# Performance work log

Measured on AMD Instinct MI355X. Metric: run time of the kernel, lower is better.

## Reference

```python
import jax, jax.numpy as jnp
import numpy as np

N = 8192
D = 256
DENSITY = 0.02  # ~164 neighbors per node


def setup_inputs() -> dict:
    key = jax.random.key(0)
    k1, k2, k3, k4 = jax.random.split(key, 4)
    inputs = jax.random.normal(k1, (N, D), dtype=jnp.float32)
    vals = jax.random.uniform(k2, (N, N), dtype=jnp.float32, minval=0.1, maxval=1.0)
    mask = jax.random.uniform(k3, (N, N), dtype=jnp.float32) < DENSITY
    adj = jnp.where(mask, vals, 0.0)
    H_v = 0.1 * jax.random.normal(k4, (D, 1), dtype=jnp.float32)
    return {"inputs": inputs, "adj": adj, "H_v": H_v}


def reference(inputs, adj, H_v):
    # scores[j] = inputs[j] . H_v  -> sparse values v_ij = adj_ij * scores[j]
    scores = jnp.squeeze(inputs @ H_v, -1)            # [N]
    mask = adj != 0.0                                  # nonzero pattern of SparseTensor
    logits = adj * scores[None, :]                     # [N, N]
    neg = jnp.asarray(jnp.finfo(logits.dtype).min, logits.dtype)
    logits = jnp.where(mask, logits, neg)
    # sparse softmax: normalize only over nonzero entries per row
    m = jnp.max(logits, axis=1, keepdims=True)
    e = jnp.where(mask, jnp.exp(logits - m), 0.0)
    s = jnp.sum(e, axis=1, keepdims=True)
    weights = e / jnp.where(s > 0, s, 1.0)             # empty rows -> all-zero weights
    # sparse_tensor_dense_matmul(weights, inputs)
    return weights @ inputs                            # [N, D]
```

## Files before the change

kernel.cpp:

```cpp
#include <hip/hip_runtime.h>

#define NN 8192
#define DD 256
#define RCAP 512

typedef float v4f __attribute__((ext_vector_type(4)));
typedef unsigned short u16x4 __attribute__((ext_vector_type(4)));

__device__ __forceinline__ unsigned short f2bf_rne(float x) {
    unsigned u = __float_as_uint(x);
    u += 0x7fffu + ((u >> 16) & 1u);
    return (unsigned short)(u >> 16);
}

__device__ __forceinline__ float4 bf4_to_f4(u16x4 u) {
    float4 r;
    r.x = __uint_as_float((unsigned)u.x << 16);
    r.y = __uint_as_float((unsigned)u.y << 16);
    r.z = __uint_as_float((unsigned)u.z << 16);
    r.w = __uint_as_float((unsigned)u.w << 16);
    return r;
}

template <bool WRITE_IB>
__global__ __launch_bounds__(256) void prep_kernel(const float* __restrict__ inputs,
                                                   const float* __restrict__ Hv,
                                                   float* __restrict__ scores,
                                                   unsigned short* __restrict__ ib) {
    int wave = threadIdx.x >> 6;
    int lane = threadIdx.x & 63;
    int row  = blockIdx.x * 4 + wave;
    float4 v = ((const float4*)(inputs + (size_t)row * DD))[lane];
    if (WRITE_IB) {
        u16x4 u;
        u.x = f2bf_rne(v.x); u.y = f2bf_rne(v.y); u.z = f2bf_rne(v.z); u.w = f2bf_rne(v.w);
        ((u16x4*)(ib + (size_t)row * DD))[lane] = u;
    }
    float4 h = ((const float4*)Hv)[lane];
    float s = v.x * h.x + v.y * h.y + v.z * h.z + v.w * h.w;
    #pragma unroll
    for (int off = 32; off > 0; off >>= 1) s += __shfl_down(s, off, 64);
    if (lane == 0) scores[row] = s;
}


__device__ __forceinline__ void process_row(const v4f a[8], int row, int tid, int lane, int wave,
                                            const float* __restrict__ scores,
                                            float2* __restrict__ csr, int* __restrict__ cnt,
                                            float2* s_ja, int* s_wsum) {
    int nz = 0;
#pragma unroll
    for (int c = 0; c < 8; ++c)
        nz += (a[c].x != 0.f) + (a[c].y != 0.f) + (a[c].z != 0.f) + (a[c].w != 0.f);

    int pre = nz;
#pragma unroll
    for (int off = 1; off < 64; off <<= 1) {
        int t = __shfl_up(pre, off, 64);
        if (lane >= off) pre += t;
    }
    if (lane == 63) s_wsum[wave] = pre;
    __syncthreads();
    int base = 0, total = 0;
#pragma unroll
    for (int w = 0; w < 4; ++w) {
        int t = s_wsum[w];
        if (w < wave) base += t;
        total += t;
    }

    int off = base + pre - nz;
#pragma unroll
    for (int c = 0; c < 8; ++c) {
        int j0 = c * 1024 + tid * 4;
        float v;
        v = a[c].x; if (v != 0.f) { if (off < RCAP) s_ja[off] = make_float2(__int_as_float(j0 + 0), v); off++; }
        v = a[c].y; if (v != 0.f) { if (off < RCAP) s_ja[off] = make_float2(__int_as_float(j0 + 1), v); off++; }
        v = a[c].z; if (v != 0.f) { if (off < RCAP) s_ja[off] = make_float2(__int_as_float(j0 + 2), v); off++; }
        v = a[c].w; if (v != 0.f) { if (off < RCAP) s_ja[off] = make_float2(__int_as_float(j0 + 3), v); off++; }
    }
    __syncthreads();

    int lim = total <= RCAP ? total : RCAP;
    for (int k = tid; k < lim; k += 256) {
        float2 ja = s_ja[k];
        int j = __float_as_int(ja.x);
        float e = __expf(ja.y * scores[j]);
        csr[(size_t)row * RCAP + k] = make_float2(ja.x, e);
    }
    if (tid == 0) cnt[row] = total;
    __syncthreads();
}

__global__ __launch_bounds__(256) void build_kernel(const float* __restrict__ adj,
                                                    const float* __restrict__ scores,
                                                    float2* __restrict__ csr,
                                                    int* __restrict__ cnt) {
    __shared__ float2 s_ja[RCAP];
    __shared__ int s_wsum[4];

    const int tid  = threadIdx.x;
    const int lane = tid & 63;
    const int wave = tid >> 6;
    const int row0 = blockIdx.x * 2;

    const v4f* p0 = (const v4f*)(adj + (size_t)row0 * NN);
    const v4f* p1 = (const v4f*)(adj + (size_t)(row0 + 1) * NN);
    v4f a0[8], a1[8];
#pragma unroll
    for (int c = 0; c < 8; ++c) a0[c] = __builtin_nontemporal_load(&p0[c * 256 + tid]);
#pragma unroll
    for (int c = 0; c < 8; ++c) a1[c] = __builtin_nontemporal_load(&p1[c * 256 + tid]);

    process_row(a0, row0,     tid, lane, wave, scores, csr, cnt, s_ja, s_wsum);
    process_row(a1, row0 + 1, tid, lane, wave, scores, csr, cnt, s_ja, s_wsum);
}


__device__ __forceinline__ void batch8(const unsigned short* __restrict__ ib,
                                       int jl, int el, int m, int lane4,
                                       float4& acc, float& ssum) {
    int js[8]; float es[8]; float4 f[8];
#pragma unroll
    for (int u = 0; u < 8; ++u) {
        js[u] = __builtin_amdgcn_readlane(jl, m + u);
        es[u] = __uint_as_float(__builtin_amdgcn_readlane(el, m + u));
    }
#pragma unroll
    for (int u = 0; u < 8; ++u)
        f[u] = bf4_to_f4(*(const u16x4*)(ib + (size_t)js[u] * DD + lane4));
#pragma unroll
    for (int u = 0; u < 8; ++u) {
        acc.x += es[u] * f[u].x; acc.y += es[u] * f[u].y;
        acc.z += es[u] * f[u].z; acc.w += es[u] * f[u].w;
        ssum  += es[u];
    }
}

__device__ void gather_pair(const float2* __restrict__ eA, int bA, int keA,
                            const float2* __restrict__ eB, int bB, int keB,
                            const unsigned short* __restrict__ ib,
                            int lane, int lane4,
                            float4& accA, float& ssA, float4& accB, float& ssB) {
    while (bA < keA || bB < keB) {
        int nA = keA - bA; nA = nA > 64 ? 64 : nA;
        int nB = keB - bB; nB = nB > 64 ? 64 : nB;
        int jlA = 0, elA = 0, jlB = 0, elB = 0;
        if (nA > 0) {
            float2 je = eA[bA + (lane < nA ? lane : 0)];
            if (lane >= nA) je.y = 0.f;
            jlA = __float_as_int(je.x); elA = __float_as_int(je.y);
        }
        if (nB > 0) {
            float2 je = eB[bB + (lane < nB ? lane : 0)];
            if (lane >= nB) je.y = 0.f;
            jlB = __float_as_int(je.x); elB = __float_as_int(je.y);
        }
        int nA8 = nA > 0 ? ((nA + 7) & ~7) : 0;
        int nB8 = nB > 0 ? ((nB + 7) & ~7) : 0;
        int mx = nA8 > nB8 ? nA8 : nB8;
        for (int m = 0; m < mx; m += 8) {
            if (m < nA8) batch8(ib, jlA, elA, m, lane4, accA, ssA);
            if (m < nB8) batch8(ib, jlB, elB, m, lane4, accB, ssB);
        }
        if (nA > 0) bA += nA;
        if (nB > 0) bB += nB;
    }
}

__device__ void slow_row(const float* __restrict__ adj, int row,
                         const float* __restrict__ scores,
                         const unsigned short* __restrict__ ib,
                         float2* s_je, int* s_cnt,
                         int tid, int lane, int lane4, int wave,
                         float4& acc, float& ssum) {
    const float* arow = adj + (size_t)row * NN;
    for (int c = 0; c < 8; ++c) {
        if (tid == 0) *s_cnt = 0;
        __syncthreads();
        float4 a = ((const float4*)(arow + c * 1024))[tid];
        int j0 = c * 1024 + tid * 4;
        float v;
        v = a.x; if (v != 0.f) { int k = atomicAdd(s_cnt, 1); s_je[k] = make_float2(__int_as_float(j0 + 0), __expf(v * scores[j0 + 0])); }
        v = a.y; if (v != 0.f) { int k = atomicAdd(s_cnt, 1); s_je[k] = make_float2(__int_as_float(j0 + 1), __expf(v * scores[j0 + 1])); }
        v = a.z; if (v != 0.f) { int k = atomicAdd(s_cnt, 1); s_je[k] = make_float2(__int_as_float(j0 + 2), __expf(v * scores[j0 + 2])); }
        v = a.w; if (v != 0.f) { int k = atomicAdd(s_cnt, 1); s_je[k] = make_float2(__int_as_float(j0 + 3), __expf(v * scores[j0 + 3])); }
        __syncthreads();
        int tc = *s_cnt;
        float4 dummy = make_float4(0.f, 0.f, 0.f, 0.f); float sdummy = 0.f;
        gather_pair(s_je, wave * tc / 4, (wave + 1) * tc / 4,
                    s_je, 0, 0, ib, lane, lane4, acc, ssum, dummy, sdummy);
        __syncthreads();
    }
}

__global__ __launch_bounds__(256) void gather_kernel(const float2* __restrict__ csr,
                                                     const int* __restrict__ cnt,
                                                     const unsigned short* __restrict__ ib,
                                                     const float* __restrict__ adj,
                                                     const float* __restrict__ scores,
                                                     float* __restrict__ out) {
    __shared__ float  s_red[2][4 * DD];
    __shared__ float  s_ss[2][4];
    __shared__ float2 s_je[1024];
    __shared__ int    s_cnt;

    const int tid   = threadIdx.x;
    const int lane  = tid & 63;
    const int wave  = tid >> 6;
    const int lane4 = lane * 4;
    const int row0  = blockIdx.x * 2;
    const int row1  = row0 + 1;

    int t0 = cnt[row0];
    int t1 = cnt[row1];
    float4 acc0 = make_float4(0.f, 0.f, 0.f, 0.f), acc1 = acc0;
    float ss0 = 0.f, ss1 = 0.f;

    if (t0 <= RCAP && t1 <= RCAP) {
        gather_pair(csr + (size_t)row0 * RCAP, wave * t0 / 4, (wave + 1) * t0 / 4,
                    csr + (size_t)row1 * RCAP, wave * t1 / 4, (wave + 1) * t1 / 4,
                    ib, lane, lane4, acc0, ss0, acc1, ss1);
    } else {
        if (t0 <= RCAP) {
            float4 d = make_float4(0.f, 0.f, 0.f, 0.f); float sd = 0.f;
            gather_pair(csr + (size_t)row0 * RCAP, wave * t0 / 4, (wave + 1) * t0 / 4,
                        csr, 0, 0, ib, lane, lane4, acc0, ss0, d, sd);
        } else {
            slow_row(adj, row0, scores, ib, s_je, &s_cnt, tid, lane, lane4, wave, acc0, ss0);
        }
        if (t1 <= RCAP) {
            float4 d = make_float4(0.f, 0.f, 0.f, 0.f); float sd = 0.f;
            gather_pair(csr + (size_t)row1 * RCAP, wave * t1 / 4, (wave + 1) * t1 / 4,
                        csr, 0, 0, ib, lane, lane4, acc1, ss1, d, sd);
        } else {
            slow_row(adj, row1, scores, ib, s_je, &s_cnt, tid, lane, lane4, wave, acc1, ss1);
        }
    }

    if (lane == 0) { s_ss[0][wave] = ss0; s_ss[1][wave] = ss1; }
    *(float4*)&s_red[0][wave * DD + lane4] = acc0;
    *(float4*)&s_red[1][wave * DD + lane4] = acc1;
    __syncthreads();
    float tot0 = s_ss[0][0] + s_ss[0][1] + s_ss[0][2] + s_ss[0][3];
    float tot1 = s_ss[1][0] + s_ss[1][1] + s_ss[1][2] + s_ss[1][3];
    float r0 = s_red[0][0 * DD + tid] + s_red[0][1 * DD + tid] + s_red[0][2 * DD + tid] + s_red[0][3 * DD + tid];
    float r1 = s_red[1][0 * DD + tid] + s_red[1][1 * DD + tid] + s_red[1][2 * DD + tid] + s_red[1][3 * DD + tid];
    out[(size_t)row0 * DD + tid] = (tot0 > 0.f) ? r0 / tot0 : 0.f;
    out[(size_t)row1 * DD + tid] = (tot1 > 0.f) ? r1 / tot1 : 0.f;
}

__global__ __launch_bounds__(256) void attn_fallback(const float* __restrict__ adj,
                                                     const float* __restrict__ inputs,
                                                     const float* __restrict__ scores,
                                                     float* __restrict__ out) {
    __shared__ int   s_j[1024];
    __shared__ float s_e[1024];
    __shared__ int   s_cnt;
    const int row = blockIdx.x;
    const int tid = threadIdx.x;
    const float* arow = adj + (size_t)row * NN;
    float acc = 0.f, ssum = 0.f;
    for (int base = 0; base < NN; base += 1024) {
        if (tid == 0) s_cnt = 0;
        __syncthreads();
        float4 a = ((const float4*)(arow + base))[tid];
        int j0 = base + tid * 4;
        if (a.x != 0.f) { int k = atomicAdd(&s_cnt, 1); s_j[k] = j0 + 0; s_e[k] = __expf(a.x * scores[j0 + 0]); }
        if (a.y != 0.f) { int k = atomicAdd(&s_cnt, 1); s_j[k] = j0 + 1; s_e[k] = __expf(a.y * scores[j0 + 1]); }
        if (a.z != 0.f) { int k = atomicAdd(&s_cnt, 1); s_j[k] = j0 + 2; s_e[k] = __expf(a.z * scores[j0 + 2]); }
        if (a.w != 0.f) { int k = atomicAdd(&s_cnt, 1); s_j[k] = j0 + 3; s_e[k] = __expf(a.w * scores[j0 + 3]); }
        __syncthreads();
        int c = s_cnt;
        for (int k = 0; k < c; ++k) {
            float e = s_e[k];
            acc  += e * inputs[(size_t)s_j[k] * DD + tid];
            ssum += e;
        }
        __syncthreads();
    }
    out[(size_t)row * DD + tid] = (ssum > 0.f) ? acc / ssum : 0.f;
}

extern "C" void kernel_launch(void* const* d_in, const int* in_sizes, int n_in,
                              void* d_out, int out_size, void* d_ws, size_t ws_size,
                              hipStream_t stream) {
    const float* inputs = (const float*)d_in[0];
    const float* adj    = (const float*)d_in[1];
    const float* Hv     = (const float*)d_in[2];
    float* out = (float*)d_out;

    char* ws = (char*)d_ws;
    float*          scores = (float*)ws;
    unsigned short* ib     = (unsigned short*)(ws + 32768);
    int*            cnt    = (int*)(ws + 32768 + (size_t)NN * DD * 2);
    float2*         csr    = (float2*)(ws + 65536 + (size_t)NN * DD * 2);

    const size_t need = 65536 + (size_t)NN * DD * 2 + (size_t)NN * RCAP * sizeof(float2);

    if (ws_size >= need) {
        prep_kernel<true><<<NN / 4, 256, 0, stream>>>(inputs, Hv, scores, ib);
        build_kernel<<<NN / 2, 256, 0, stream>>>(adj, scores, csr, cnt);
        gather_kernel<<<NN / 2, 256, 0, stream>>>(csr, cnt, ib, adj, scores, out);
    } else {
        prep_kernel<false><<<NN / 4, 256, 0, stream>>>(inputs, Hv, scores, nullptr);
        attn_fallback<<<NN, 256, 0, stream>>>(adj, inputs, scores, out);
    }
}
```

Before: 399.4 us.

## Fuse CSR build and gather into one per-row kernel using shared-memory neighbor lists

Merges the separate build and gather kernels into a single kernel with one block per row. Each block compacts the row's nonzeros and their exp weights into shared memory and gathers bf16 neighbor rows from there directly, so the global CSR buffer is never written or read back. The gather now has each half-wave load 8 bf16 values per lane from a different neighbor, and the shared-memory capacity is raised to 1024 entries. In exchange there is a larger shared-memory reduction, each block handles only one row instead of two, and there is less overlap between the adjacency stream and the gather.

```diff
diff --git a/kernel.cpp b/kernel.cpp
--- a/kernel.cpp
+++ b/kernel.cpp
@@ -2,24 +2,16 @@
 
 #define NN 8192
 #define DD 256
-#define RCAP 512
+#define RCAP 1024
 
 typedef float v4f __attribute__((ext_vector_type(4)));
 typedef unsigned short u16x4 __attribute__((ext_vector_type(4)));
+typedef unsigned short u16x8 __attribute__((ext_vector_type(8)));
 
 __device__ __forceinline__ unsigned short f2bf_rne(float x) {
     unsigned u = __float_as_uint(x);
     u += 0x7fffu + ((u >> 16) & 1u);
     return (unsigned short)(u >> 16);
-}
-
-__device__ __forceinline__ float4 bf4_to_f4(u16x4 u) {
-    float4 r;
-    r.x = __uint_as_float((unsigned)u.x << 16);
-    r.y = __uint_as_float((unsigned)u.y << 16);
-    r.z = __uint_as_float((unsigned)u.z << 16);
-    r.w = __uint_as_float((unsigned)u.w << 16);
-    return r;
 }
 
 template <bool WRITE_IB>
@@ -43,16 +35,81 @@
     if (lane == 0) scores[row] = s;
 }
 
-
-__device__ __forceinline__ void process_row(const v4f a[8], int row, int tid, int lane, int wave,
-                                            const float* __restrict__ scores,
-                                            float2* __restrict__ csr, int* __restrict__ cnt,
-                                            float2* s_ja, int* s_wsum) {
+__device__ __forceinline__ void batch8x2(const unsigned short* __restrict__ ib,
+                                         int jl, int el, int m, int sel, int lane8,
+                                         float4& accL, float4& accH, float& ssum) {
+    int js[8]; float es[8];
+#pragma unroll
+    for (int u = 0; u < 8; ++u) {
+        js[u] = __builtin_amdgcn_readlane(jl, m + u);
+        es[u] = __uint_as_float(__builtin_amdgcn_readlane(el, m + u));
+    }
+    u16x8 g[4];
+#pragma unroll
+    for (int p = 0; p < 4; ++p) {
+        int j = sel ? js[2 * p + 1] : js[2 * p];
+        g[p] = *(const u16x8*)(ib + (size_t)j * DD + lane8);
+    }
+#pragma unroll
+    for (int p = 0; p < 4; ++p) {
+        float e = sel ? es[2 * p + 1] : es[2 * p];
+        float4 lo, hi;
+        lo.x = __uint_as_float((unsigned)g[p][0] << 16);
+        lo.y = __uint_as_float((unsigned)g[p][1] << 16);
+        lo.z = __uint_as_float((unsigned)g[p][2] << 16);
+        lo.w = __uint_as_float((unsigned)g[p][3] << 16);
+        hi.x = __uint_as_float((unsigned)g[p][4] << 16);
+        hi.y = __uint_as_float((unsigned)g[p][5] << 16);
+        hi.z = __uint_as_float((unsigned)g[p][6] << 16);
+        hi.w = __uint_as_float((unsigned)g[p][7] << 16);
+        accL.x += e * lo.x; accL.y += e * lo.y; accL.z += e * lo.z; accL.w += e * lo.w;
+        accH.x += e * hi.x; accH.y += e * hi.y; accH.z += e * hi.z; accH.w += e * hi.w;
+        ssum += e;
+    }
+}
+
+__device__ __forceinline__ void gather_range(const float2* __restrict__ s_je, int b, int ke,
+                                             const unsigned short* __restrict__ ib, int lane,
+                                             float4& accL, float4& accH, float& ssum) {
+    const int sel   = lane >> 5;
+    const int lane8 = (lane & 31) * 8;
+    while (b < ke) {
+        int n = ke - b; n = n > 64 ? 64 : n;
+        float2 je = s_je[b + (lane < n ? lane : 0)];
+        if (lane >= n) je.y = 0.f;
+        int jl = __float_as_int(je.x);
+        int el = __float_as_int(je.y);
+        int n8 = (n + 7) & ~7;
+        for (int m = 0; m < n8; m += 8)
+            batch8x2(ib, jl, el, m, sel, lane8, accL, accH, ssum);
+        b += n;
+    }
+}
+
+__global__ __launch_bounds__(256) void fused_kernel(const float* __restrict__ adj,
+                                                    const float* __restrict__ scores,
+                                                    const unsigned short* __restrict__ ib,
+                                                    float* __restrict__ out) {
+    __shared__ float2 s_je[RCAP];
+    __shared__ float  s_red[8 * DD];
+    __shared__ float  s_ss[8];
+    __shared__ int    s_wsum[4];
+    __shared__ int    s_cnt;
+
+    const int tid  = threadIdx.x;
+    const int lane = tid & 63;
+    const int wave = tid >> 6;
+    const int row  = blockIdx.x;
+
+    const v4f* p = (const v4f*)(adj + (size_t)row * NN);
+    v4f a[8];
+#pragma unroll
+    for (int c = 0; c < 8; ++c) a[c] = __builtin_nontemporal_load(&p[c * 256 + tid]);
+
     int nz = 0;
 #pragma unroll
     for (int c = 0; c < 8; ++c)
         nz += (a[c].x != 0.f) + (a[c].y != 0.f) + (a[c].z != 0.f) + (a[c].w != 0.f);
-
     int pre = nz;
 #pragma unroll
     for (int off = 1; off < 64; off <<= 1) {
@@ -69,185 +126,52 @@
         total += t;
     }
 
-    int off = base + pre - nz;
-#pragma unroll
-    for (int c = 0; c < 8; ++c) {
-        int j0 = c * 1024 + tid * 4;
-        float v;
-        v = a[c].x; if (v != 0.f) { if (off < RCAP) s_ja[off] = make_float2(__int_as_float(j0 + 0), v); off++; }
-        v = a[c].y; if (v != 0.f) { if (off < RCAP) s_ja[off] = make_float2(__int_as_float(j0 + 1), v); off++; }
-        v = a[c].z; if (v != 0.f) { if (off < RCAP) s_ja[off] = make_float2(__int_as_float(j0 + 2), v); off++; }
-        v = a[c].w; if (v != 0.f) { if (off < RCAP) s_ja[off] = make_float2(__int_as_float(j0 + 3), v); off++; }
-    }
+    float4 accL = make_float4(0.f, 0.f, 0.f, 0.f), accH = accL;
+    float ssum = 0.f;
+
+    if (total <= RCAP) {
+        int off = base + pre - nz;
+#pragma unroll
+        for (int c = 0; c < 8; ++c) {
+            int j0 = c * 1024 + tid * 4;
+            float v;
+            v = a[c].x; if (v != 0.f) { s_je[off] = make_float2(__int_as_float(j0 + 0), __expf(v * scores[j0 + 0])); off++; }
+            v = a[c].y; if (v != 0.f) { s_je[off] = make_float2(__int_as_float(j0 + 1), __expf(v * scores[j0 + 1])); off++; }
+            v = a[c].z; if (v != 0.f) { s_je[off] = make_float2(__int_as_float(j0 + 2), __expf(v * scores[j0 + 2])); off++; }
+            v = a[c].w; if (v != 0.f) { s_je[off] = make_float2(__int_as_float(j0 + 3), __expf(v * scores[j0 + 3])); off++; }
+        }
+        __syncthreads();
+        gather_range(s_je, wave * total / 4, (wave + 1) * total / 4, ib, lane, accL, accH, ssum);
+    } else {
+        for (int c = 0; c < 8; ++c) {
+            if (tid == 0) s_cnt = 0;
+            __syncthreads();
+            int j0 = c * 1024 + tid * 4;
+            float v;
+            v = a[c].x; if (v != 0.f) { int k = atomicAdd(&s_cnt, 1); s_je[k] = make_float2(__int_as_float(j0 + 0), __expf(v * scores[j0 + 0])); }
+            v = a[c].y; if (v != 0.f) { int k = atomicAdd(&s_cnt, 1); s_je[k] = make_float2(__int_as_float(j0 + 1), __expf(v * scores[j0 + 1])); }
+            v = a[c].z; if (v != 0.f) { int k = atomicAdd(&s_cnt, 1); s_je[k] = make_float2(__int_as_float(j0 + 2), __expf(v * scores[j0 + 2])); }
+            v = a[c].w; if (v != 0.f) { int k = atomicAdd(&s_cnt, 1); s_je[k] = make_float2(__int_as_float(j0 + 3), __expf(v * scores[j0 + 3])); }
+            __syncthreads();
+            int tc = s_cnt;
+            gather_range(s_je, wave * tc / 4, (wave + 1) * tc / 4, ib, lane, accL, accH, ssum);
+            __syncthreads();
+        }
+    }
+
+    const int half = wave * 2 + (lane >> 5);
+    const int l8   = (lane & 31) * 8;
+    if ((lane & 31) == 0) s_ss[half] = ssum;
+    *(float4*)&s_red[half * DD + l8]     = accL;
+    *(float4*)&s_red[half * DD + l8 + 4] = accH;
     __syncthreads();
-
-    int lim = total <= RCAP ? total : RCAP;
-    for (int k = tid; k < lim; k += 256) {
-        float2 ja = s_ja[k];
-        int j = __float_as_int(ja.x);
-        float e = __expf(ja.y * scores[j]);
-        csr[(size_t)row * RCAP + k] = make_float2(ja.x, e);
-    }
-    if (tid == 0) cnt[row] = total;
-    __syncthreads();
-}
-
-__global__ __launch_bounds__(256) void build_kernel(const float* __restrict__ adj,
-                                                    const float* __restrict__ scores,
-                                                    float2* __restrict__ csr,
-                                                    int* __restrict__ cnt) {
-    __shared__ float2 s_ja[RCAP];
-    __shared__ int s_wsum[4];
-
-    const int tid  = threadIdx.x;
-    const int lane = tid & 63;
-    const int wave = tid >> 6;
-    const int row0 = blockIdx.x * 2;
-
-    const v4f* p0 = (const v4f*)(adj + (size_t)row0 * NN);
-    const v4f* p1 = (const v4f*)(adj + (size_t)(row0 + 1) * NN);
-    v4f a0[8], a1[8];
-#pragma unroll
-    for (int c = 0; c < 8; ++c) a0[c] = __builtin_nontemporal_load(&p0[c * 256 + tid]);
-#pragma unroll
-    for (int c = 0; c < 8; ++c) a1[c] = __builtin_nontemporal_load(&p1[c * 256 + tid]);
-
-    process_row(a0, row0,     tid, lane, wave, scores, csr, cnt, s_ja, s_wsum);
-    process_row(a1, row0 + 1, tid, lane, wave, scores, csr, cnt, s_ja, s_wsum);
-}
-
-
-__device__ __forceinline__ void batch8(const unsigned short* __restrict__ ib,
-                                       int jl, int el, int m, int lane4,
-                                       float4& acc, float& ssum) {
-    int js[8]; float es[8]; float4 f[8];
-#pragma unroll
-    for (int u = 0; u < 8; ++u) {
-        js[u] = __builtin_amdgcn_readlane(jl, m + u);
-        es[u] = __uint_as_float(__builtin_amdgcn_readlane(el, m + u));
-    }
-#pragma unroll
-    for (int u = 0; u < 8; ++u)
-        f[u] = bf4_to_f4(*(const u16x4*)(ib + (size_t)js[u] * DD + lane4));
-#pragma unroll
-    for (int u = 0; u < 8; ++u) {
-        acc.x += es[u] * f[u].x; acc.y += es[u] * f[u].y;
-        acc.z += es[u] * f[u].z; acc.w += es[u] * f[u].w;
-        ssum  += es[u];
-    }
-}
-
-__device__ void gather_pair(const float2* __restrict__ eA, int bA, int keA,
-                            const float2* __restrict__ eB, int bB, int keB,
-                            const unsigned short* __restrict__ ib,
-                            int lane, int lane4,
-                            float4& accA, float& ssA, float4& accB, float& ssB) {
-    while (bA < keA || bB < keB) {
-        int nA = keA - bA; nA = nA > 64 ? 64 : nA;
-        int nB = keB - bB; nB = nB > 64 ? 64 : nB;
-        int jlA = 0, elA = 0, jlB = 0, elB = 0;
-        if (nA > 0) {
-            float2 je = eA[bA + (lane < nA ? lane : 0)];
-            if (lane >= nA) je.y = 0.f;
-            jlA = __float_as_int(je.x); elA = __float_as_int(je.y);
-        }
-        if (nB > 0) {
-            float2 je = eB[bB + (lane < nB ? lane : 0)];
-            if (lane >= nB) je.y = 0.f;
-            jlB = __float_as_int(je.x); elB = __float_as_int(je.y);
-        }
-        int nA8 = nA > 0 ? ((nA + 7) & ~7) : 0;
-        int nB8 = nB > 0 ? ((nB + 7) & ~7) : 0;
-        int mx = nA8 > nB8 ? nA8 : nB8;
-        for (int m = 0; m < mx; m += 8) {
-            if (m < nA8) batch8(ib, jlA, elA, m, lane4, accA, ssA);
-            if (m < nB8) batch8(ib, jlB, elB, m, lane4, accB, ssB);
-        }
-        if (nA > 0) bA += nA;
-        if (nB > 0) bB += nB;
-    }
-}
-
-__device__ void slow_row(const float* __restrict__ adj, int row,
-                         const float* __restrict__ scores,
-                         const unsigned short* __restrict__ ib,
-                         float2* s_je, int* s_cnt,
-                         int tid, int lane, int lane4, int wave,
-                         float4& acc, float& ssum) {
-    const float* arow = adj + (size_t)row * NN;
-    for (int c = 0; c < 8; ++c) {
-        if (tid == 0) *s_cnt = 0;
-        __syncthreads();
-        float4 a = ((const float4*)(arow + c * 1024))[tid];
-        int j0 = c * 1024 + tid * 4;
-        float v;
-        v = a.x; if (v != 0.f) { int k = atomicAdd(s_cnt, 1); s_je[k] = make_float2(__int_as_float(j0 + 0), __expf(v * scores[j0 + 0])); }
-        v = a.y; if (v != 0.f) { int k = atomicAdd(s_cnt, 1); s_je[k] = make_float2(__int_as_float(j0 + 1), __expf(v * scores[j0 + 1])); }
-        v = a.z; if (v != 0.f) { int k = atomicAdd(s_cnt, 1); s_je[k] = make_float2(__int_as_float(j0 + 2), __expf(v * scores[j0 + 2])); }
-        v = a.w; if (v != 0.f) { int k = atomicAdd(s_cnt, 1); s_je[k] = make_float2(__int_as_float(j0 + 3), __expf(v * scores[j0 + 3])); }
-        __syncthreads();
-        int tc = *s_cnt;
-        float4 dummy = make_float4(0.f, 0.f, 0.f, 0.f); float sdummy = 0.f;
-        gather_pair(s_je, wave * tc / 4, (wave + 1) * tc / 4,
-                    s_je, 0, 0, ib, lane, lane4, acc, ssum, dummy, sdummy);
-        __syncthreads();
-    }
-}
-
-__global__ __launch_bounds__(256) void gather_kernel(const float2* __restrict__ csr,
-                                                     const int* __restrict__ cnt,
-                                                     const unsigned short* __restrict__ ib,
-                                                     const float* __restrict__ adj,
-                                                     const float* __restrict__ scores,
-                                                     float* __restrict__ out) {
-    __shared__ float  s_red[2][4 * DD];
-    __shared__ float  s_ss[2][4];
-    __shared__ float2 s_je[1024];
-    __shared__ int    s_cnt;
-
-    const int tid   = threadIdx.x;
-    const int lane  = tid & 63;
-    const int wave  = tid >> 6;
-    const int lane4 = lane * 4;
-    const int row0  = blockIdx.x * 2;
-    const int row1  = row0 + 1;
-
-    int t0 = cnt[row0];
-    int t1 = cnt[row1];
-    float4 acc0 = make_float4(0.f, 0.f, 0.f, 0.f), acc1 = acc0;
-    float ss0 = 0.f, ss1 = 0.f;
-
-    if (t0 <= RCAP && t1 <= RCAP) {
-        gather_pair(csr + (size_t)row0 * RCAP, wave * t0 / 4, (wave + 1) * t0 / 4,
-                    csr + (size_t)row1 * RCAP, wave * t1 / 4, (wave + 1) * t1 / 4,
-                    ib, lane, lane4, acc0, ss0, acc1, ss1);
-    } else {
-        if (t0 <= RCAP) {
-            float4 d = make_float4(0.f, 0.f, 0.f, 0.f); float sd = 0.f;
-            gather_pair(csr + (size_t)row0 * RCAP, wave * t0 / 4, (wave + 1) * t0 / 4,
-                        csr, 0, 0, ib, lane, lane4, acc0, ss0, d, sd);
-        } else {
-            slow_row(adj, row0, scores, ib, s_je, &s_cnt, tid, lane, lane4, wave, acc0, ss0);
-        }
-        if (t1 <= RCAP) {
-            float4 d = make_float4(0.f, 0.f, 0.f, 0.f); float sd = 0.f;
-            gather_pair(csr + (size_t)row1 * RCAP, wave * t1 / 4, (wave + 1) * t1 / 4,
-                        csr, 0, 0, ib, lane, lane4, acc1, ss1, d, sd);
-        } else {
-            slow_row(adj, row1, scores, ib, s_je, &s_cnt, tid, lane, lane4, wave, acc1, ss1);
-        }
-    }
-
-    if (lane == 0) { s_ss[0][wave] = ss0; s_ss[1][wave] = ss1; }
-    *(float4*)&s_red[0][wave * DD + lane4] = acc0;
-    *(float4*)&s_red[1][wave * DD + lane4] = acc1;
-    __syncthreads();
-    float tot0 = s_ss[0][0] + s_ss[0][1] + s_ss[0][2] + s_ss[0][3];
-    float tot1 = s_ss[1][0] + s_ss[1][1] + s_ss[1][2] + s_ss[1][3];
-    float r0 = s_red[0][0 * DD + tid] + s_red[0][1 * DD + tid] + s_red[0][2 * DD + tid] + s_red[0][3 * DD + tid];
-    float r1 = s_red[1][0 * DD + tid] + s_red[1][1 * DD + tid] + s_red[1][2 * DD + tid] + s_red[1][3 * DD + tid];
-    out[(size_t)row0 * DD + tid] = (tot0 > 0.f) ? r0 / tot0 : 0.f;
-    out[(size_t)row1 * DD + tid] = (tot1 > 0.f) ? r1 / tot1 : 0.f;
+    float tot = 0.f;
+#pragma unroll
+    for (int i = 0; i < 8; ++i) tot += s_ss[i];
+    float r = 0.f;
+#pragma unroll
+    for (int i = 0; i < 8; ++i) r += s_red[i * DD + tid];
+    out[(size_t)row * DD + tid] = (tot > 0.f) ? r / tot : 0.f;
 }
 
 __global__ __launch_bounds__(256) void attn_fallback(const float* __restrict__ adj,
@@ -293,15 +217,12 @@
     char* ws = (char*)d_ws;
     float*          scores = (float*)ws;
     unsigned short* ib     = (unsigned short*)(ws + 32768);
-    int*            cnt    = (int*)(ws + 32768 + (size_t)NN * DD * 2);
-    float2*         csr    = (float2*)(ws + 65536 + (size_t)NN * DD * 2);
-
-    const size_t need = 65536 + (size_t)NN * DD * 2 + (size_t)NN * RCAP * sizeof(float2);
+
+    const size_t need = 32768 + (size_t)NN * DD * 2;
 
     if (ws_size >= need) {
         prep_kernel<true><<<NN / 4, 256, 0, stream>>>(inputs, Hv, scores, ib);
-        build_kernel<<<NN / 2, 256, 0, stream>>>(adj, scores, csr, cnt);
-        gather_kernel<<<NN / 2, 256, 0, stream>>>(csr, cnt, ib, adj, scores, out);
+        fused_kernel<<<NN, 256, 0, stream>>>(adj, scores, ib, out);
     } else {
         prep_kernel<false><<<NN / 4, 256, 0, stream>>>(inputs, Hv, scores, nullptr);
         attn_fallback<<<NN, 256, 0, stream>>>(adj, inputs, scores, out);
```

Result: slower. 409.1 us (+2.4%).
